# Performance work log

Hardware: AMD Instinct MI355X
Metric: run time of the kernel (lower is better)

## Reference

```python
import jax, jax.numpy as jnp
import numpy as np


def setup_inputs() -> dict:
    key = jax.random.key(0)
    k1, k2 = jax.random.split(key)
    N, C = 2_000_000, 5  # N points, 3 coords + C feature channels
    range_min = jnp.array([0.0, -39.68, -3.0], jnp.float32)
    range_max = jnp.array([69.12, 39.68, 1.0], jnp.float32)
    voxel_size = jnp.array([0.16, 0.16, 4.0], jnp.float32)  # KITTI pillars -> 432x496x1 grid
    xyz = jax.random.uniform(k1, (N, 3), jnp.float32) * (range_max - range_min) + range_min
    feats = jax.random.normal(k2, (N, C), jnp.float32)
    points_feats = jnp.concatenate([xyz, feats], axis=1)
    return {"points_feats": points_feats, "voxel_size": voxel_size,
            "range_min": range_min, "range_max": range_max,
            "max_num_points": 64, "max_voxels": 60000}


def reference(points_feats, voxel_size, range_min, range_max, max_num_points, max_voxels):
    """PointPillars voxelization: hash points into pillars, build dense [V, P, D] tensor.

    Returns fixed-size (padded) outputs for jit-compatibility:
      out_voxels     [max_voxels, max_num_points, D]  zero-padded point feats per voxel
      out_coords     [max_voxels, 3]                  integer voxel coords, order [z, y, x]
      out_num_points [max_voxels]                     points per voxel (0 for unused slots)
    Voxels are ordered canonically by ascending linear cell index; points keep their
    original relative order inside a voxel (stable sort), matching ragged_to_dense+gather
    semantics with zero padding (feats row-0 zero trick in the original).
    """
    N, D = points_feats.shape
    pts = points_feats[:, :3]
    grid = jnp.round((range_max - range_min) / voxel_size).astype(jnp.int32)  # [gx, gy, gz]
    vox = jnp.floor((pts - range_min) / voxel_size).astype(jnp.int32)         # [N, 3] (x, y, z)
    valid = jnp.all((vox >= 0) & (vox < grid), axis=1)
    n_cells = grid[0] * grid[1] * grid[2]
    lin = (vox[:, 2] * grid[1] + vox[:, 1]) * grid[0] + vox[:, 0]
    lin = jnp.where(valid, lin, n_cells)  # invalid points sort to the end

    order = jnp.argsort(lin)  # stable: preserves point order within a voxel
    slin = lin[order]
    svalid = valid[order]
    svox = vox[order]
    sfeats = points_feats[order]

    idx = jnp.arange(N, dtype=jnp.int32)
    is_new = jnp.concatenate([jnp.ones((1,), bool), slin[1:] != slin[:-1]])
    is_start = is_new & svalid                      # first point of each occupied voxel
    voxel_id = jnp.cumsum(is_start.astype(jnp.int32)) - 1
    run_start = jax.lax.cummax(jnp.where(is_start, idx, 0))
    rank = idx - run_start                          # slot of point inside its voxel

    keep = svalid & (voxel_id < max_voxels) & (rank < max_num_points)
    vi = jnp.where(keep, voxel_id, max_voxels)      # out-of-range index -> dropped
    ri = jnp.where(keep, rank, 0)

    out_voxels = jnp.zeros((max_voxels, max_num_points, D), points_feats.dtype)
    out_voxels = out_voxels.at[vi, ri].set(sfeats, mode="drop")

    ci = jnp.where(is_start & (voxel_id < max_voxels), voxel_id, max_voxels)
    out_coords = jnp.zeros((max_voxels, 3), jnp.int32).at[ci].set(svox[:, ::-1], mode="drop")  # [z,y,x]

    out_num_points = jax.ops.segment_sum(keep.astype(jnp.int32), vi,
                                         num_segments=max_voxels + 1)[:max_voxels]
    return out_voxels, out_coords, out_num_points
```

## Files before the change

kernel.cpp:

```cpp
#include <hip/hip_runtime.h>


constexpr int MAXV    = 60000;
constexpr int MAXP    = 64;
constexpr int DF      = 8;
constexpr int NCMAX   = 432 * 496;
constexpr int NB      = NCMAX / 256;
constexpr int EMCAP   = 256;
constexpr int CSTRIDE = 4;
constexpr int CSR_CAP = 1000000;

struct Geom { float rm[3], ir[3]; int g[3]; };

__device__ __forceinline__ Geom load_geom(const float* __restrict__ vs,
                                          const float* __restrict__ rmin,
                                          const float* __restrict__ rmax) {
  Geom ge;
#pragma unroll
  for (int a = 0; a < 3; ++a) {
    ge.rm[a] = rmin[a];
    ge.ir[a] = 1.0f / vs[a];
    ge.g[a]  = (int)rintf((rmax[a] - rmin[a]) * ge.ir[a]);
  }
  return ge;
}

__device__ __forceinline__ bool cell_of(float4 p, const Geom& ge, int& lin) {
  float c[3] = { p.x, p.y, p.z };
  int v[3]; bool ok = true;
#pragma unroll
  for (int a = 0; a < 3; ++a) {
    float q = floorf((c[a] - ge.rm[a]) * ge.ir[a]);
    v[a] = (int)q;
    ok = ok && (q >= 0.0f) && (v[a] < ge.g[a]);
  }
  lin = (v[2] * ge.g[1] + v[1]) * ge.g[0] + v[0];
  return ok && lin >= 0 && lin < NCMAX;
}

__global__ void k_count(const float* __restrict__ pts, int N,
                        const float* __restrict__ vs, const float* __restrict__ rmin,
                        const float* __restrict__ rmax,
                        int* __restrict__ counts, unsigned int* __restrict__ linslot) {
  int i = blockIdx.x * blockDim.x + threadIdx.x;
  if (i >= N) return;
  Geom ge = load_geom(vs, rmin, rmax);
  float4 p = *(const float4*)(pts + (size_t)i * DF);
  unsigned int pack = 0xFFFFFFFFu;
  int lin;
  if (cell_of(p, ge, lin)) {
    int slot = atomicAdd(counts + (size_t)lin * CSTRIDE, 1);
    pack = ((unsigned int)lin << 8) | (unsigned int)(slot < 255 ? slot : 255);
  }
  linslot[i] = pack;
}

__global__ void k_bsumA(const int* __restrict__ counts, int* __restrict__ bsA) {
  __shared__ int s[256];
  int t = threadIdx.x, i = blockIdx.x * 256 + t;
  s[t] = (counts[(size_t)i * CSTRIDE] > 0) ? 1 : 0;
  __syncthreads();
  for (int off = 128; off > 0; off >>= 1) { if (t < off) s[t] += s[t + off]; __syncthreads(); }
  if (t == 0) bsA[blockIdx.x] = s[0];
}

__global__ void k_scan(int* __restrict__ b, int n) {
  __shared__ int s[1024];
  int t = threadIdx.x;
  int v = (t < n) ? b[t] : 0;
  s[t] = v; __syncthreads();
  for (int off = 1; off < 1024; off <<= 1) {
    int x = (t >= off) ? s[t - off] : 0;
    __syncthreads(); s[t] += x; __syncthreads();
  }
  if (t < n) b[t] = s[t] - v;
}

__global__ void k_bsumB(const int* __restrict__ counts, const int* __restrict__ bsA,
                        int* __restrict__ bsB) {
  __shared__ int s[256];
  int t = threadIdx.x, i = blockIdx.x * 256 + t;
  int cnt = counts[(size_t)i * CSTRIDE];
  int f = (cnt > 0) ? 1 : 0;
  s[t] = f; __syncthreads();
  for (int off = 1; off < 256; off <<= 1) {
    int x = (t >= off) ? s[t - off] : 0;
    __syncthreads(); s[t] += x; __syncthreads();
  }
  int vid = bsA[blockIdx.x] + s[t] - f;
  int alloc = (f && vid < MAXV) ? min(cnt, EMCAP) : 0;
  __syncthreads();
  s[t] = alloc; __syncthreads();
  for (int off = 128; off > 0; off >>= 1) { if (t < off) s[t] += s[t + off]; __syncthreads(); }
  if (t == 0) bsB[blockIdx.x] = s[0];
}

__global__ void k_final(const int* __restrict__ counts, const int* __restrict__ bsA,
                        const int* __restrict__ bsB,
                        int* __restrict__ cellbase, int* __restrict__ vbase,
                        int* __restrict__ vcnt,
                        float* __restrict__ out_coords, float* __restrict__ out_nump) {
  __shared__ int so[256], sk[256];
  int t = threadIdx.x, i = blockIdx.x * 256 + t;
  int cnt = counts[(size_t)i * CSTRIDE];
  int f = (cnt > 0) ? 1 : 0;
  so[t] = f; __syncthreads();
  for (int off = 1; off < 256; off <<= 1) {
    int x = (t >= off) ? so[t - off] : 0;
    __syncthreads(); so[t] += x; __syncthreads();
  }
  int vid = bsA[blockIdx.x] + so[t] - f;
  int alloc = (f && vid < MAXV) ? min(cnt, EMCAP) : 0;
  sk[t] = alloc; __syncthreads();
  for (int off = 1; off < 256; off <<= 1) {
    int x = (t >= off) ? sk[t - off] : 0;
    __syncthreads(); sk[t] += x; __syncthreads();
  }
  int base = bsB[blockIdx.x] + sk[t] - alloc;
  if (alloc > 0) {
    cellbase[i] = base;
    vbase[vid] = base;
    vcnt[vid] = alloc;
    int x = i % 432, rest = i / 432, y = rest % 496, z = rest / 496;
    out_coords[(size_t)vid * 3 + 0] = (float)z;
    out_coords[(size_t)vid * 3 + 1] = (float)y;
    out_coords[(size_t)vid * 3 + 2] = (float)x;
    out_nump[vid] = (float)(cnt < MAXP ? cnt : MAXP);
  } else {
    cellbase[i] = -1;
  }
}

__global__ void k_scatter(const unsigned int* __restrict__ linslot, int N,
                          const int* __restrict__ cellbase, int* __restrict__ csr) {
  int t4 = (blockIdx.x * blockDim.x + threadIdx.x) * 4;
  if (t4 + 3 >= N) {
    for (int i = t4; i < N; ++i) {
      unsigned int pk = linslot[i];
      if (pk == 0xFFFFFFFFu) continue;
      int lin = (int)(pk >> 8), sl = (int)(pk & 255u);
      int b = cellbase[lin];
      if (b < 0 || sl >= EMCAP) continue;
      int pos = b + sl;
      if (pos < CSR_CAP) csr[pos] = i;
    }
    return;
  }
  uint4 pk4 = *(const uint4*)(linslot + t4);
  unsigned int pk[4] = { pk4.x, pk4.y, pk4.z, pk4.w };
#pragma unroll
  for (int j = 0; j < 4; ++j) {
    if (pk[j] == 0xFFFFFFFFu) continue;
    int lin = (int)(pk[j] >> 8), sl = (int)(pk[j] & 255u);
    int b = cellbase[lin];
    if (b < 0 || sl >= EMCAP) continue;
    int pos = b + sl;
    if (pos < CSR_CAP) csr[pos] = t4 + j;
  }
}

__global__ void __launch_bounds__(64)
k_emit(const float* __restrict__ pts,
       const int* __restrict__ vbase, const int* __restrict__ vcnt,
       const int* __restrict__ csr, float* __restrict__ out_vox) {
  int v = blockIdx.x, t = threadIdx.x;
  int kf = vcnt[v];
  __shared__ int sidx[EMCAP];
  __shared__ int sorted[MAXP];
  sorted[t] = -1;
  int base = vbase[v];
  for (int j = t; j < kf; j += 64) sidx[j] = csr[base + j];
  __syncthreads();
  for (int e = t; e < kf; e += 64) {
    int my = sidx[e], rank = 0;
    for (int j = 0; j < kf; ++j) rank += (sidx[j] < my) ? 1 : 0;
    if (rank < MAXP) sorted[rank] = my;
  }
  __syncthreads();
  int pi = sorted[t];
  float4 a = make_float4(0.f, 0.f, 0.f, 0.f);
  float4 b = a;
  if (pi >= 0) {
    const float4* src = (const float4*)(pts + (size_t)pi * DF);
    a = src[0]; b = src[1];
  }
  float4* dst = (float4*)(out_vox + ((size_t)v * MAXP + t) * DF);
  dst[0] = a;
  dst[1] = b;
}

extern "C" void kernel_launch(void* const* d_in, const int* in_sizes, int n_in,
                              void* d_out, int out_size, void* d_ws, size_t ws_size,
                              hipStream_t stream) {
  const float* pts  = (const float*)d_in[0];
  const float* vs   = (const float*)d_in[1];
  const float* rmin = (const float*)d_in[2];
  const float* rmax = (const float*)d_in[3];
  const int N = in_sizes[0] / DF;

  char* ws = (char*)d_ws;
  int* counts          = (int*)(ws);
  int* vcnt            = (int*)(ws +  3428352);
  int* vbase           = (int*)(ws +  3668352);
  int* bsA             = (int*)(ws +  3908352);
  int* bsB             = (int*)(ws +  3912448);
  int* cellbase        = (int*)(ws +  3916544);
  unsigned int* linslot= (unsigned int*)(ws + 4773632);
  int* csr             = (int*)(ws + 12773632);

  float* out_vox    = (float*)d_out;
  float* out_coords = (float*)d_out + (size_t)MAXV * MAXP * DF;
  float* out_nump   = out_coords + (size_t)MAXV * 3;

  hipMemsetAsync(ws, 0, 3908352, stream);
  hipMemsetAsync((void*)out_coords, 0, (size_t)MAXV * 4 * 4, stream);

  const int nb1 = (N + 255) / 256;
  const int nb4 = (N + 1023) / 1024;
  k_count  <<<nb1, 256, 0, stream>>>(pts, N, vs, rmin, rmax, counts, linslot);
  k_bsumA  <<<NB, 256, 0, stream>>>(counts, bsA);
  k_scan   <<<1, 1024, 0, stream>>>(bsA, NB);
  k_bsumB  <<<NB, 256, 0, stream>>>(counts, bsA, bsB);
  k_scan   <<<1, 1024, 0, stream>>>(bsB, NB);
  k_final  <<<NB, 256, 0, stream>>>(counts, bsA, bsB, cellbase, vbase, vcnt,
                                    out_coords, out_nump);
  k_scatter<<<nb4, 256, 0, stream>>>(linslot, N, cellbase, csr);
  k_emit   <<<MAXV, 64, 0, stream>>>(pts, vbase, vcnt, csr, out_vox);
}
```

Measured before the change: 280.3 us.

## Count only low cells first, add conditional fallback pass, fuse block-prefix scans

New measurement: 365.3 us. 30.3% more time.

```diff
diff --git a/kernel.cpp b/kernel.cpp
--- a/kernel.cpp
+++ b/kernel.cpp
@@ -9,6 +9,9 @@
 constexpr int EMCAP   = 256;
 constexpr int CSTRIDE = 4;
 constexpr int CSR_CAP = 1000000;
+constexpr int THRESH  = 73728;
+
+typedef float __attribute__((ext_vector_type(4))) f32x4;
 
 struct Geom { float rm[3], ir[3]; int g[3]; };
 
@@ -41,18 +44,43 @@
 __global__ void k_count(const float* __restrict__ pts, int N,
                         const float* __restrict__ vs, const float* __restrict__ rmin,
                         const float* __restrict__ rmax,
-                        int* __restrict__ counts, unsigned int* __restrict__ linslot) {
+                        int* __restrict__ counts, unsigned int* __restrict__ linslot,
+                        int* __restrict__ occ) {
   int i = blockIdx.x * blockDim.x + threadIdx.x;
   if (i >= N) return;
   Geom ge = load_geom(vs, rmin, rmax);
   float4 p = *(const float4*)(pts + (size_t)i * DF);
   unsigned int pack = 0xFFFFFFFFu;
   int lin;
-  if (cell_of(p, ge, lin)) {
+  if (cell_of(p, ge, lin) && lin < THRESH) {
     int slot = atomicAdd(counts + (size_t)lin * CSTRIDE, 1);
+    if (slot == 0) atomicAdd(occ + (blockIdx.x & 15), 1);
     pack = ((unsigned int)lin << 8) | (unsigned int)(slot < 255 ? slot : 255);
   }
   linslot[i] = pack;
+}
+
+__global__ void k_fallback(const float* __restrict__ pts, int N,
+                           const float* __restrict__ vs, const float* __restrict__ rmin,
+                           const float* __restrict__ rmax,
+                           int* __restrict__ counts, unsigned int* __restrict__ linslot,
+                           const int* __restrict__ occ) {
+  int o = 0;
+#pragma unroll
+  for (int j = 0; j < 16; ++j) o += occ[j];
+  if (o >= MAXV) return;
+  Geom ge = load_geom(vs, rmin, rmax);
+  int t4 = (blockIdx.x * blockDim.x + threadIdx.x) * 4;
+  for (int j = 0; j < 4; ++j) {
+    int i = t4 + j;
+    if (i >= N) break;
+    float4 p = *(const float4*)(pts + (size_t)i * DF);
+    int lin;
+    if (cell_of(p, ge, lin) && lin >= THRESH) {
+      int slot = atomicAdd(counts + (size_t)lin * CSTRIDE, 1);
+      linslot[i] = ((unsigned int)lin << 8) | (unsigned int)(slot < 255 ? slot : 255);
+    }
+  }
 }
 
 __global__ void k_bsumA(const int* __restrict__ counts, int* __restrict__ bsA) {
@@ -64,22 +92,16 @@
   if (t == 0) bsA[blockIdx.x] = s[0];
 }
 
-__global__ void k_scan(int* __restrict__ b, int n) {
-  __shared__ int s[1024];
-  int t = threadIdx.x;
-  int v = (t < n) ? b[t] : 0;
-  s[t] = v; __syncthreads();
-  for (int off = 1; off < 1024; off <<= 1) {
-    int x = (t >= off) ? s[t - off] : 0;
-    __syncthreads(); s[t] += x; __syncthreads();
-  }
-  if (t < n) b[t] = s[t] - v;
-}
-
 __global__ void k_bsumB(const int* __restrict__ counts, const int* __restrict__ bsA,
                         int* __restrict__ bsB) {
+  __shared__ int sp[256];
   __shared__ int s[256];
-  int t = threadIdx.x, i = blockIdx.x * 256 + t;
+  int t = threadIdx.x, b = blockIdx.x, i = b * 256 + t;
+  int pa = 0;
+  for (int j = t; j < b; j += 256) pa += bsA[j];
+  sp[t] = pa; __syncthreads();
+  for (int off = 128; off > 0; off >>= 1) { if (t < off) sp[t] += sp[t + off]; __syncthreads(); }
+  int prefixA = sp[0];
   int cnt = counts[(size_t)i * CSTRIDE];
   int f = (cnt > 0) ? 1 : 0;
   s[t] = f; __syncthreads();
@@ -87,7 +109,7 @@
     int x = (t >= off) ? s[t - off] : 0;
     __syncthreads(); s[t] += x; __syncthreads();
   }
-  int vid = bsA[blockIdx.x] + s[t] - f;
+  int vid = prefixA + s[t] - f;
   int alloc = (f && vid < MAXV) ? min(cnt, EMCAP) : 0;
   __syncthreads();
   s[t] = alloc; __syncthreads();
@@ -100,8 +122,16 @@
                         int* __restrict__ cellbase, int* __restrict__ vbase,
                         int* __restrict__ vcnt,
                         float* __restrict__ out_coords, float* __restrict__ out_nump) {
-  __shared__ int so[256], sk[256];
-  int t = threadIdx.x, i = blockIdx.x * 256 + t;
+  __shared__ int sp[256], so[256], sk[256];
+  int t = threadIdx.x, b = blockIdx.x, i = b * 256 + t;
+  int pa = 0, pb = 0;
+  for (int j = t; j < b; j += 256) { pa += bsA[j]; pb += bsB[j]; }
+  sp[t] = pa; __syncthreads();
+  for (int off = 128; off > 0; off >>= 1) { if (t < off) sp[t] += sp[t + off]; __syncthreads(); }
+  int prefixA = sp[0]; __syncthreads();
+  sp[t] = pb; __syncthreads();
+  for (int off = 128; off > 0; off >>= 1) { if (t < off) sp[t] += sp[t + off]; __syncthreads(); }
+  int prefixB = sp[0];
   int cnt = counts[(size_t)i * CSTRIDE];
   int f = (cnt > 0) ? 1 : 0;
   so[t] = f; __syncthreads();
@@ -109,14 +139,14 @@
     int x = (t >= off) ? so[t - off] : 0;
     __syncthreads(); so[t] += x; __syncthreads();
   }
-  int vid = bsA[blockIdx.x] + so[t] - f;
+  int vid = prefixA + so[t] - f;
   int alloc = (f && vid < MAXV) ? min(cnt, EMCAP) : 0;
   sk[t] = alloc; __syncthreads();
   for (int off = 1; off < 256; off <<= 1) {
     int x = (t >= off) ? sk[t - off] : 0;
     __syncthreads(); sk[t] += x; __syncthreads();
   }
-  int base = bsB[blockIdx.x] + sk[t] - alloc;
+  int base = prefixB + sk[t] - alloc;
   if (alloc > 0) {
     cellbase[i] = base;
     vbase[vid] = base;
@@ -178,15 +208,15 @@
   }
   __syncthreads();
   int pi = sorted[t];
-  float4 a = make_float4(0.f, 0.f, 0.f, 0.f);
-  float4 b = a;
+  f32x4 a = {0.f, 0.f, 0.f, 0.f};
+  f32x4 b = {0.f, 0.f, 0.f, 0.f};
   if (pi >= 0) {
-    const float4* src = (const float4*)(pts + (size_t)pi * DF);
+    const f32x4* src = (const f32x4*)(pts + (size_t)pi * DF);
     a = src[0]; b = src[1];
   }
-  float4* dst = (float4*)(out_vox + ((size_t)v * MAXP + t) * DF);
-  dst[0] = a;
-  dst[1] = b;
+  f32x4* dst = (f32x4*)(out_vox + ((size_t)v * MAXP + t) * DF);
+  __builtin_nontemporal_store(a, dst);
+  __builtin_nontemporal_store(b, dst + 1);
 }
 
 extern "C" void kernel_launch(void* const* d_in, const int* in_sizes, int n_in,
@@ -202,28 +232,28 @@
   int* counts          = (int*)(ws);
   int* vcnt            = (int*)(ws +  3428352);
   int* vbase           = (int*)(ws +  3668352);
-  int* bsA             = (int*)(ws +  3908352);
-  int* bsB             = (int*)(ws +  3912448);
-  int* cellbase        = (int*)(ws +  3916544);
-  unsigned int* linslot= (unsigned int*)(ws + 4773632);
-  int* csr             = (int*)(ws + 12773632);
+  int* occ             = (int*)(ws +  3908352);
+  int* bsA             = (int*)(ws +  3908416);
+  int* bsB             = (int*)(ws +  3912512);
+  int* cellbase        = (int*)(ws +  3916608);
+  unsigned int* linslot= (unsigned int*)(ws + 4773696);
+  int* csr             = (int*)(ws + 12773696);
 
   float* out_vox    = (float*)d_out;
   float* out_coords = (float*)d_out + (size_t)MAXV * MAXP * DF;
   float* out_nump   = out_coords + (size_t)MAXV * 3;
 
-  hipMemsetAsync(ws, 0, 3908352, stream);
+  hipMemsetAsync(ws, 0, 3908416, stream);
   hipMemsetAsync((void*)out_coords, 0, (size_t)MAXV * 4 * 4, stream);
 
   const int nb1 = (N + 255) / 256;
   const int nb4 = (N + 1023) / 1024;
-  k_count  <<<nb1, 256, 0, stream>>>(pts, N, vs, rmin, rmax, counts, linslot);
-  k_bsumA  <<<NB, 256, 0, stream>>>(counts, bsA);
-  k_scan   <<<1, 1024, 0, stream>>>(bsA, NB);
-  k_bsumB  <<<NB, 256, 0, stream>>>(counts, bsA, bsB);
-  k_scan   <<<1, 1024, 0, stream>>>(bsB, NB);
-  k_final  <<<NB, 256, 0, stream>>>(counts, bsA, bsB, cellbase, vbase, vcnt,
-                                    out_coords, out_nump);
-  k_scatter<<<nb4, 256, 0, stream>>>(linslot, N, cellbase, csr);
-  k_emit   <<<MAXV, 64, 0, stream>>>(pts, vbase, vcnt, csr, out_vox);
-}
+  k_count   <<<nb1, 256, 0, stream>>>(pts, N, vs, rmin, rmax, counts, linslot, occ);
+  k_fallback<<<nb4, 256, 0, stream>>>(pts, N, vs, rmin, rmax, counts, linslot, occ);
+  k_bsumA   <<<NB, 256, 0, stream>>>(counts, bsA);
+  k_bsumB   <<<NB, 256, 0, stream>>>(counts, bsA, bsB);
+  k_final   <<<NB, 256, 0, stream>>>(counts, bsA, bsB, cellbase, vbase, vcnt,
+                                     out_coords, out_nump);
+  k_scatter <<<nb4, 256, 0, stream>>>(linslot, N, cellbase, csr);
+  k_emit    <<<MAXV, 64, 0, stream>>>(pts, vbase, vcnt, csr, out_vox);
+}
```
